# Kernel optimization log

Hardware: AMD Instinct MI355X
Metric: run time of the kernel (lower is better)

The kernel has to match this reference:

```python
import math
import jax, jax.numpy as jnp
import numpy as np

B, SQ, SK, D, H = 4, 2048, 2048, 1024, 16
HD = D // H  # 64


def setup_inputs() -> dict:
    key = jax.random.key(0)
    k1, k2, k3, k4, k5 = jax.random.split(key, 5)
    scale = 1.0 / math.sqrt(D)
    return {
        "hidden_states": jax.random.normal(k1, (B, SQ, D), dtype=jnp.float32),
        "encoder_hidden_states": jax.random.normal(k2, (B, SK, D), dtype=jnp.float32),
        "Wq": jax.random.normal(k3, (D, D), dtype=jnp.float32) * scale,
        "Wk": jax.random.normal(k4, (D, D), dtype=jnp.float32) * scale,
        "Wv": jax.random.normal(k5, (D, D), dtype=jnp.float32) * scale,
    }


def reference(hidden_states, encoder_hidden_states, Wq, Wk, Wv):
    # Linear (bias=False): y = x @ W^T, then split heads -> [B, H, S, HD]
    def split_heads(x, S):
        return x.reshape(B, S, H, HD).transpose(0, 2, 1, 3)

    q = split_heads(hidden_states @ Wq.T, SQ)
    k = split_heads(encoder_hidden_states @ Wk.T, SK)
    v = split_heads(encoder_hidden_states @ Wv.T, SK)

    scores = jnp.einsum("bhqd,bhkd->bhqk", q, k) / math.sqrt(HD)
    probs = jax.nn.softmax(scores, axis=-1)  # no mask, dropout p=0
    ctx = jnp.einsum("bhqk,bhkd->bhqd", probs, v)
    # merge heads -> [B, SQ, D]
    return ctx.transpose(0, 2, 1, 3).reshape(B, SQ, D)
```

## Files before the change

### kernel.cpp

```cpp
#include <hip/hip_runtime.h>
#include <hip/hip_bf16.h>

typedef unsigned short u16;
typedef unsigned int u32;
typedef __attribute__((ext_vector_type(8))) short bf16x8;
typedef __attribute__((ext_vector_type(4))) float f32x4;

#define MFMA32(a, b, c) __builtin_amdgcn_mfma_f32_16x16x32_bf16(a, b, c, 0, 0, 0)

__device__ __forceinline__ float fexp2(float x) { return __builtin_amdgcn_exp2f(x); }

__device__ __forceinline__ u16 f2bf(float f) {
  u32 u = __float_as_uint(f);
  u += 0x7fffu + ((u >> 16) & 1u);
  return (u16)(u >> 16);
}
__device__ __forceinline__ u32 pack2rn(float a, float b) {
  return (u32)f2bf(a) | ((u32)f2bf(b) << 16);
}
__device__ __forceinline__ bf16x8 cvt8(const float4 a, const float4 b) {
  union { bf16x8 v; u32 p[4]; } r;
  r.p[0] = pack2rn(a.x, a.y); r.p[1] = pack2rn(a.z, a.w);
  r.p[2] = pack2rn(b.x, b.y); r.p[3] = pack2rn(b.z, b.w);
  return r.v;
}

__device__ __forceinline__ u32 cvtpk(float lo, float hi) {
  u32 r;
  asm("v_cvt_pk_bf16_f32 %0, %1, %2" : "=v"(r) : "v"(lo), "v"(hi));
  return r;
}
__device__ __forceinline__ void pl32swap(u32& a, u32& b) {
  asm("v_permlane32_swap_b32 %0, %1" : "+v"(a), "+v"(b));
}
__device__ __forceinline__ void pl16swap(u32& a, u32& b) {
  asm("v_permlane16_swap_b32 %0, %1" : "+v"(a), "+v"(b));
}

__device__ __forceinline__ void async_copy16(const void* g, void* l) {
  __builtin_amdgcn_global_load_lds(
      (const __attribute__((address_space(1))) unsigned int*)g,
      (__attribute__((address_space(3))) unsigned int*)l, 16, 0, 0);
}

__global__ __launch_bounds__(256) void cvt_bf16(
    const float* __restrict__ s0, const float* __restrict__ s1,
    const float* __restrict__ s2, const float* __restrict__ s3,
    const float* __restrict__ s4,
    u16* __restrict__ d0, u16* __restrict__ d1, u16* __restrict__ d2,
    u16* __restrict__ d3, u16* __restrict__ d4) {
  const int z = blockIdx.z;
  const float* s = (z == 0) ? s0 : (z == 1) ? s1 : (z == 2) ? s2 : (z == 3) ? s3 : s4;
  u16* d = (z == 0) ? d0 : (z == 1) ? d1 : (z == 2) ? d2 : (z == 3) ? d3 : d4;
  const int n8 = ((z < 2) ? (8192 * 1024) : (1024 * 1024)) / 8;
  const int stride = gridDim.x * 256;
  for (int i = blockIdx.x * 256 + threadIdx.x; i < n8; i += stride) {
    const float4 a = *(const float4*)(s + (size_t)i * 8);
    const float4 b = *(const float4*)(s + (size_t)i * 8 + 4);
    *(bf16x8*)(d + (size_t)i * 8) = cvt8(a, b);
  }
}

__global__ __launch_bounds__(256) void proj_gemm_bf(
    const u16* __restrict__ hb, const u16* __restrict__ eb,
    const u16* __restrict__ wb,
    u16* __restrict__ qb, u16* __restrict__ kb, u16* __restrict__ vt) {
  const int lin = blockIdx.x;
  const int swz = (lin & 7) * 192 + (lin >> 3);
  const int z = swz >> 9;
  const int rem = swz & 511;
  const int m0 = (rem >> 3) * 128;
  const int n0 = (rem & 7) * 128;
  const u16* Ag = (z == 0) ? hb : eb;
  const u16* Bg = wb + (size_t)z * 1024 * 1024;
  __shared__ __attribute__((aligned(16))) u16 Al[128 * 64];
  __shared__ __attribute__((aligned(16))) u16 Bl[128 * 64];
  const int tid = threadIdx.x;
  const int w = tid >> 6, lane = tid & 63;
  const int wm = w >> 1, wn = w & 1;
  const int l15 = lane & 15, quad = lane >> 4;
  const int lr = lane >> 3;
  const int cs8 = ((lane & 7) ^ lr) * 8;
  const int rsw = (l15 & 7) << 3;

  const u16* Ap = Ag + (size_t)(m0 + w * 32 + lr) * 1024 + cs8;
  const u16* Bp = Bg + (size_t)(n0 + w * 32 + lr) * 1024 + cs8;

  f32x4 acc[4][4] = {};

  for (int k0 = 0; k0 < 1024; k0 += 64) {
    __syncthreads();
#pragma unroll
    for (int j = 0; j < 4; j++) {
      async_copy16(Ap + (size_t)j * 8 * 1024 + k0, &Al[(w * 32 + j * 8) * 64]);
      async_copy16(Bp + (size_t)j * 8 * 1024 + k0, &Bl[(w * 32 + j * 8) * 64]);
    }
    __syncthreads();
#pragma unroll
    for (int ks = 0; ks < 2; ks++) {
      bf16x8 af[4], bfr[4];
#pragma unroll
      for (int t = 0; t < 4; t++) {
        af[t] = *(const bf16x8*)&Al[(wm * 64 + t * 16 + l15) * 64 +
                                    ((ks * 32 + quad * 8) ^ rsw)];
        bfr[t] = *(const bf16x8*)&Bl[(wn * 64 + t * 16 + l15) * 64 +
                                     ((ks * 32 + quad * 8) ^ rsw)];
      }
#pragma unroll
      for (int mt = 0; mt < 4; mt++)
#pragma unroll
        for (int nt = 0; nt < 4; nt++)
          acc[mt][nt] = MFMA32(af[mt], bfr[nt], acc[mt][nt]);
    }
  }

  if (z < 2) {
    u16* C = (z == 0) ? qb : kb;
    const float sc = (z == 0) ? 0.18033688011112042f : 1.0f;
#pragma unroll
    for (int mt = 0; mt < 4; mt++)
#pragma unroll
      for (int nt = 0; nt < 4; nt++) {
        const int col = n0 + wn * 64 + nt * 16 + l15;
#pragma unroll
        for (int rr = 0; rr < 4; rr++) {
          const int rowm = m0 + wm * 64 + mt * 16 + quad * 4 + rr;
          C[(size_t)rowm * 1024 + col] = f2bf(acc[mt][nt][rr] * sc);
        }
      }
  } else {
    const int b = m0 >> 11;
#pragma unroll
    for (int mt = 0; mt < 4; mt++) {
      const int key = (m0 & 2047) + wm * 64 + mt * 16 + quad * 4;
#pragma unroll
      for (int nt = 0; nt < 4; nt++) {
        const int n = n0 + wn * 64 + nt * 16 + l15;
        const int h = n >> 6, hd = n & 63;
        uint2 v;
        v.x = pack2rn(acc[mt][nt][0], acc[mt][nt][1]);
        v.y = pack2rn(acc[mt][nt][2], acc[mt][nt][3]);
        *(uint2*)&vt[((size_t)((b * 16 + h) * 64 + hd)) * 2048 + key] = v;
      }
    }
  }
}

__global__ __launch_bounds__(256) void proj_gemm_f32(
    const float* __restrict__ hs, const float* __restrict__ ehs,
    const float* __restrict__ wq, const float* __restrict__ wk,
    const float* __restrict__ wv,
    u16* __restrict__ qb, u16* __restrict__ kb, u16* __restrict__ vt) {
  const int z = blockIdx.z;
  const float* Ag = (z == 0) ? hs : ehs;
  const float* Bg = (z == 0) ? wq : ((z == 1) ? wk : wv);
  const int m0 = blockIdx.y * 128;
  const int n0 = blockIdx.x * 128;
  __shared__ __attribute__((aligned(16))) u16 Al[128 * 40];
  __shared__ __attribute__((aligned(16))) u16 Bl[128 * 40];
  const int tid = threadIdx.x;
  const int w = tid >> 6, lane = tid & 63;
  const int wm = w >> 1, wn = w & 1;
  const int l15 = lane & 15, quad = lane >> 4;
  const int srow = lane >> 2, sch = lane & 3;
  const int r0 = w * 32 + srow, r1 = r0 + 16;

  const float* Ap0 = Ag + (size_t)(m0 + r0) * 1024 + sch * 8;
  const float* Ap1 = Ag + (size_t)(m0 + r1) * 1024 + sch * 8;
  const float* Bp0 = Bg + (size_t)(n0 + r0) * 1024 + sch * 8;
  const float* Bp1 = Bg + (size_t)(n0 + r1) * 1024 + sch * 8;

  f32x4 acc[4][4] = {};

  for (int k0 = 0; k0 < 1024; k0 += 32) {
    const float4 a0l = *(const float4*)(Ap0 + k0), a0h = *(const float4*)(Ap0 + k0 + 4);
    const float4 a1l = *(const float4*)(Ap1 + k0), a1h = *(const float4*)(Ap1 + k0 + 4);
    const float4 b0l = *(const float4*)(Bp0 + k0), b0h = *(const float4*)(Bp0 + k0 + 4);
    const float4 b1l = *(const float4*)(Bp1 + k0), b1h = *(const float4*)(Bp1 + k0 + 4);
    __syncthreads();
    *(bf16x8*)&Al[r0 * 40 + sch * 8] = cvt8(a0l, a0h);
    *(bf16x8*)&Al[r1 * 40 + sch * 8] = cvt8(a1l, a1h);
    *(bf16x8*)&Bl[r0 * 40 + sch * 8] = cvt8(b0l, b0h);
    *(bf16x8*)&Bl[r1 * 40 + sch * 8] = cvt8(b1l, b1h);
    __syncthreads();
    bf16x8 af[4], bfr[4];
#pragma unroll
    for (int t = 0; t < 4; t++) {
      af[t] = *(const bf16x8*)&Al[(wm * 64 + t * 16 + l15) * 40 + quad * 8];
      bfr[t] = *(const bf16x8*)&Bl[(wn * 64 + t * 16 + l15) * 40 + quad * 8];
    }
#pragma unroll
    for (int mt = 0; mt < 4; mt++)
#pragma unroll
      for (int nt = 0; nt < 4; nt++)
        acc[mt][nt] = MFMA32(af[mt], bfr[nt], acc[mt][nt]);
  }

  if (z < 2) {
    u16* C = (z == 0) ? qb : kb;
    const float sc = (z == 0) ? 0.18033688011112042f : 1.0f;
#pragma unroll
    for (int mt = 0; mt < 4; mt++)
#pragma unroll
      for (int nt = 0; nt < 4; nt++) {
        const int col = n0 + wn * 64 + nt * 16 + l15;
#pragma unroll
        for (int rr = 0; rr < 4; rr++) {
          const int rowm = m0 + wm * 64 + mt * 16 + quad * 4 + rr;
          C[(size_t)rowm * 1024 + col] = f2bf(acc[mt][nt][rr] * sc);
        }
      }
  } else {
    const int b = m0 >> 11;
#pragma unroll
    for (int mt = 0; mt < 4; mt++) {
      const int key = (m0 & 2047) + wm * 64 + mt * 16 + quad * 4;
#pragma unroll
      for (int nt = 0; nt < 4; nt++) {
        const int n = n0 + wn * 64 + nt * 16 + l15;
        const int h = n >> 6, hd = n & 63;
        uint2 v;
        v.x = pack2rn(acc[mt][nt][0], acc[mt][nt][1]);
        v.y = pack2rn(acc[mt][nt][2], acc[mt][nt][3]);
        *(uint2*)&vt[((size_t)((b * 16 + h) * 64 + hd)) * 2048 + key] = v;
      }
    }
  }
}

__global__ __launch_bounds__(256, 3) void attn_fwd(
    const u16* __restrict__ qb, const u16* __restrict__ kb,
    const u16* __restrict__ vt, float* __restrict__ out) {
  const int lin = blockIdx.x;
  const int swz = (lin & 7) * 128 + (lin >> 3);
  const int bh = swz >> 4;
  const int b = bh >> 4, h = bh & 15;
  const int q0 = (swz & 15) * 128;
  const int tid = threadIdx.x;
  const int w = tid >> 6, lane = tid & 63;
  const int l15 = lane & 15, quad = lane >> 4;

  __shared__ __attribute__((aligned(16))) u16 Kl[2][64 * 64];
  __shared__ __attribute__((aligned(16))) u16 Vl[2][64 * 64];

  const int wq = w * 32;
  bf16x8 qf[2][2];
#pragma unroll
  for (int nt = 0; nt < 2; nt++)
#pragma unroll
    for (int ks = 0; ks < 2; ks++)
      qf[nt][ks] = *(const bf16x8*)&qb[((size_t)(b * 2048 + q0 + wq + nt * 16 + l15)) * 1024 +
                                       h * 64 + ks * 32 + quad * 8];

  f32x4 o[4][2] = {};
  f32x4 lacc[2] = {};
  const f32x4 z4 = {0.f, 0.f, 0.f, 0.f};
  union { bf16x8 v; u32 p[4]; } one_;
  one_.p[0] = one_.p[1] = one_.p[2] = one_.p[3] = 0x3F803F80u;
  const bf16x8 ones = one_.v;

  const int rsw = (l15 & 7) << 3;
  const int lr = lane >> 3;
  const int cs8 = ((lane & 7) ^ lr) * 8;
  const u16* Kp = kb + ((size_t)(b * 2048 + w * 16 + lr)) * 1024 + h * 64 + cs8;
  const u16* Vp = vt + ((size_t)((b * 16 + h) * 64 + w * 16 + lr)) * 2048 + cs8;

#pragma unroll
  for (int j = 0; j < 2; j++) {
    async_copy16(Kp + (size_t)j * 8 * 1024, &Kl[0][(w * 16 + j * 8) * 64]);
    async_copy16(Vp + (size_t)j * 8 * 2048, &Vl[0][(w * 16 + j * 8) * 64]);
  }

  for (int t = 0; t < 32; ++t) {
    const int cur = t & 1;
    __syncthreads();
    if (t < 31) {
      const size_t ko = (size_t)(t + 1) * 64;
#pragma unroll
      for (int j = 0; j < 2; j++) {
        async_copy16(Kp + (ko + (size_t)j * 8) * 1024,
                     &Kl[cur ^ 1][(w * 16 + j * 8) * 64]);
        async_copy16(Vp + (size_t)j * 8 * 2048 + ko,
                     &Vl[cur ^ 1][(w * 16 + j * 8) * 64]);
      }
    }
    const u16* Kc = Kl[cur];
    const u16* Vc = Vl[cur];

    f32x4 s[4][2];
#pragma unroll
    for (int mt = 0; mt < 4; mt++) {
      const bf16x8 kf = *(const bf16x8*)&Kc[(mt * 16 + l15) * 64 + ((quad * 8) ^ rsw)];
      s[mt][0] = MFMA32(kf, qf[0][0], z4);
      s[mt][1] = MFMA32(kf, qf[1][0], z4);
    }
#pragma unroll
    for (int mt = 0; mt < 4; mt++) {
      const bf16x8 kf =
          *(const bf16x8*)&Kc[(mt * 16 + l15) * 64 + ((32 + quad * 8) ^ rsw)];
      s[mt][0] = MFMA32(kf, qf[0][1], s[mt][0]);
      s[mt][1] = MFMA32(kf, qf[1][1], s[mt][1]);
    }

#pragma unroll
    for (int mt = 0; mt < 4; mt++)
#pragma unroll
      for (int nt = 0; nt < 2; nt++)
#pragma unroll
        for (int rr = 0; rr < 4; rr++)
          s[mt][nt][rr] = fexp2(s[mt][nt][rr]);

#pragma unroll
    for (int kt = 0; kt < 2; kt++) {
      bf16x8 pf[2];
#pragma unroll
      for (int nt = 0; nt < 2; nt++) {
        u32 r00 = cvtpk(s[2 * kt][nt][0], s[2 * kt][nt][1]);
        u32 r01 = cvtpk(s[2 * kt][nt][2], s[2 * kt][nt][3]);
        u32 r10 = cvtpk(s[2 * kt + 1][nt][0], s[2 * kt + 1][nt][1]);
        u32 r11 = cvtpk(s[2 * kt + 1][nt][2], s[2 * kt + 1][nt][3]);
        pl32swap(r00, r10);
        pl32swap(r01, r11);
        pl16swap(r00, r10);
        pl16swap(r01, r11);
        union { bf16x8 v; u32 p[4]; } u;
        u.p[0] = r00; u.p[1] = r01; u.p[2] = r10; u.p[3] = r11;
        pf[nt] = u.v;
      }
      lacc[0] = MFMA32(ones, pf[0], lacc[0]);
      lacc[1] = MFMA32(ones, pf[1], lacc[1]);
#pragma unroll
      for (int ht = 0; ht < 4; ht++) {
        const bf16x8 vf =
            *(const bf16x8*)&Vc[(ht * 16 + l15) * 64 + ((kt * 32 + quad * 8) ^ rsw)];
        o[ht][0] = MFMA32(vf, pf[0], o[ht][0]);
        o[ht][1] = MFMA32(vf, pf[1], o[ht][1]);
      }
    }
  }

#pragma unroll
  for (int nt = 0; nt < 2; nt++) {
    const float rl = 1.0f / lacc[nt][0];
    const size_t rowOff = ((size_t)(b * 2048 + q0 + wq + nt * 16 + l15)) * 1024 + h * 64;
#pragma unroll
    for (int ht = 0; ht < 4; ht++) {
      float4 v;
      v.x = o[ht][nt][0] * rl;
      v.y = o[ht][nt][1] * rl;
      v.z = o[ht][nt][2] * rl;
      v.w = o[ht][nt][3] * rl;
      *(float4*)&out[rowOff + ht * 16 + quad * 4] = v;
    }
  }
}

extern "C" void kernel_launch(void* const* d_in, const int* in_sizes, int n_in,
                              void* d_out, int out_size, void* d_ws, size_t ws_size,
                              hipStream_t stream) {
  const float* hs  = (const float*)d_in[0];
  const float* ehs = (const float*)d_in[1];
  const float* wqp = (const float*)d_in[2];
  const float* wkp = (const float*)d_in[3];
  const float* wvp = (const float*)d_in[4];
  const size_t M8 = (size_t)8192 * 1024;
  u16* qb = (u16*)d_ws;
  u16* kb = qb + M8;
  u16* vt = kb + M8;
  float* ob = (float*)d_out;

  const size_t need = (3 * M8 + 2 * M8 + 3 * (size_t)1024 * 1024) * 2;
  if (ws_size >= need) {
    u16* hb = vt + M8;
    u16* eb = hb + M8;
    u16* wb = eb + M8;
    dim3 gc(512, 1, 5);
    cvt_bf16<<<gc, dim3(256), 0, stream>>>(hs, ehs, wqp, wkp, wvp,
                                           hb, eb, wb, wb + M8 / 8, wb + M8 / 4);
    proj_gemm_bf<<<dim3(1536), dim3(256), 0, stream>>>(hb, eb, wb, qb, kb, vt);
  } else {
    dim3 gg(8, 64, 3);
    proj_gemm_f32<<<gg, dim3(256), 0, stream>>>(hs, ehs, wqp, wkp, wvp, qb, kb, vt);
  }
  attn_fwd<<<dim3(1024), dim3(256), 0, stream>>>(qb, kb, vt, ob);
}
```

Baseline: 249.4 us.

## Double-buffer projection GEMM and use explicit vmcnt waits with MFMA priority

The projection GEMM moves from single-buffered LDS tiles with two syncthreads per k-step to a double-buffered prefetch pipeline, so the next tile's global-to-LDS copy overlaps the current MFMA work. Both the GEMM and the attention loop replace __syncthreads with raw s_barrier plus explicit s_waitcnt vmcnt counts, so only the older copies are waited on. The attention MFMA sections are wrapped in s_setprio to favour matrix issue across waves. The changes double the GEMM's LDS use, which may cut occupancy, and depend on hand-counted vmcnt values being correct.

```diff
diff --git a/kernel.cpp b/kernel.cpp
--- a/kernel.cpp
+++ b/kernel.cpp
@@ -73,8 +73,8 @@
   const int n0 = (rem & 7) * 128;
   const u16* Ag = (z == 0) ? hb : eb;
   const u16* Bg = wb + (size_t)z * 1024 * 1024;
-  __shared__ __attribute__((aligned(16))) u16 Al[128 * 64];
-  __shared__ __attribute__((aligned(16))) u16 Bl[128 * 64];
+  __shared__ __attribute__((aligned(16))) u16 Al[2][128 * 64];
+  __shared__ __attribute__((aligned(16))) u16 Bl[2][128 * 64];
   const int tid = threadIdx.x;
   const int w = tid >> 6, lane = tid & 63;
   const int wm = w >> 1, wn = w & 1;
@@ -88,23 +88,40 @@
 
   f32x4 acc[4][4] = {};
 
-  for (int k0 = 0; k0 < 1024; k0 += 64) {
-    __syncthreads();
-#pragma unroll
-    for (int j = 0; j < 4; j++) {
-      async_copy16(Ap + (size_t)j * 8 * 1024 + k0, &Al[(w * 32 + j * 8) * 64]);
-      async_copy16(Bp + (size_t)j * 8 * 1024 + k0, &Bl[(w * 32 + j * 8) * 64]);
-    }
-    __syncthreads();
+#pragma unroll
+  for (int j = 0; j < 4; j++) {
+    async_copy16(Ap + (size_t)j * 8 * 1024, &Al[0][(w * 32 + j * 8) * 64]);
+    async_copy16(Bp + (size_t)j * 8 * 1024, &Bl[0][(w * 32 + j * 8) * 64]);
+  }
+
+  for (int t = 0; t < 16; ++t) {
+    const int cur = t & 1;
+    __builtin_amdgcn_s_barrier();
+    __builtin_amdgcn_sched_barrier(0);
+    if (t < 15) {
+      const int k0 = (t + 1) * 64;
+#pragma unroll
+      for (int j = 0; j < 4; j++) {
+        async_copy16(Ap + (size_t)j * 8 * 1024 + k0,
+                     &Al[cur ^ 1][(w * 32 + j * 8) * 64]);
+        async_copy16(Bp + (size_t)j * 8 * 1024 + k0,
+                     &Bl[cur ^ 1][(w * 32 + j * 8) * 64]);
+      }
+      asm volatile("s_waitcnt vmcnt(8)" ::: "memory");
+    } else {
+      asm volatile("s_waitcnt vmcnt(0)" ::: "memory");
+    }
+    __builtin_amdgcn_s_barrier();
+    __builtin_amdgcn_sched_barrier(0);
 #pragma unroll
     for (int ks = 0; ks < 2; ks++) {
       bf16x8 af[4], bfr[4];
 #pragma unroll
-      for (int t = 0; t < 4; t++) {
-        af[t] = *(const bf16x8*)&Al[(wm * 64 + t * 16 + l15) * 64 +
-                                    ((ks * 32 + quad * 8) ^ rsw)];
-        bfr[t] = *(const bf16x8*)&Bl[(wn * 64 + t * 16 + l15) * 64 +
-                                     ((ks * 32 + quad * 8) ^ rsw)];
+      for (int t4 = 0; t4 < 4; t4++) {
+        af[t4] = *(const bf16x8*)&Al[cur][(wm * 64 + t4 * 16 + l15) * 64 +
+                                         ((ks * 32 + quad * 8) ^ rsw)];
+        bfr[t4] = *(const bf16x8*)&Bl[cur][(wn * 64 + t4 * 16 + l15) * 64 +
+                                          ((ks * 32 + quad * 8) ^ rsw)];
       }
 #pragma unroll
       for (int mt = 0; mt < 4; mt++)
@@ -273,7 +290,8 @@
 
   for (int t = 0; t < 32; ++t) {
     const int cur = t & 1;
-    __syncthreads();
+    __builtin_amdgcn_s_barrier();
+    __builtin_amdgcn_sched_barrier(0);
     if (t < 31) {
       const size_t ko = (size_t)(t + 1) * 64;
 #pragma unroll
@@ -283,11 +301,17 @@
         async_copy16(Vp + (size_t)j * 8 * 2048 + ko,
                      &Vl[cur ^ 1][(w * 16 + j * 8) * 64]);
       }
-    }
+      asm volatile("s_waitcnt vmcnt(4)" ::: "memory");
+    } else {
+      asm volatile("s_waitcnt vmcnt(0)" ::: "memory");
+    }
+    __builtin_amdgcn_s_barrier();
+    __builtin_amdgcn_sched_barrier(0);
     const u16* Kc = Kl[cur];
     const u16* Vc = Vl[cur];
 
     f32x4 s[4][2];
+    __builtin_amdgcn_s_setprio(1);
 #pragma unroll
     for (int mt = 0; mt < 4; mt++) {
       const bf16x8 kf = *(const bf16x8*)&Kc[(mt * 16 + l15) * 64 + ((quad * 8) ^ rsw)];
@@ -301,6 +325,7 @@
       s[mt][0] = MFMA32(kf, qf[0][1], s[mt][0]);
       s[mt][1] = MFMA32(kf, qf[1][1], s[mt][1]);
     }
+    __builtin_amdgcn_s_setprio(0);
 
 #pragma unroll
     for (int mt = 0; mt < 4; mt++)
@@ -327,6 +352,7 @@
         u.p[0] = r00; u.p[1] = r01; u.p[2] = r10; u.p[3] = r11;
         pf[nt] = u.v;
       }
+      __builtin_amdgcn_s_setprio(1);
       lacc[0] = MFMA32(ones, pf[0], lacc[0]);
       lacc[1] = MFMA32(ones, pf[1], lacc[1]);
 #pragma unroll
@@ -336,6 +362,7 @@
         o[ht][0] = MFMA32(vf, pf[0], o[ht][0]);
         o[ht][1] = MFMA32(vf, pf[1], o[ht][1]);
       }
+      __builtin_amdgcn_s_setprio(0);
     }
   }
 
```

Measured after the change: 255.9 us. +2.6%, slower.

## Fuse fp32-to-bf16 activation conversion into projection GEMM and tune attention barriers

Applied to the files above, without the earlier changes.

The separate conversion pass over hidden_states and encoder_hidden_states is removed. The projection GEMM now reads fp32 activations directly, converts them in registers and stores them swizzled into LDS, prefetching the next K-tile into registers. The attention loop replaces __syncthreads with explicit barriers, partial vmcnt waits and setprio around MFMA blocks to improve overlap. This saves a full write and read of the bf16 activation copies, but the GEMM now reads twice as many A bytes per tile and converts the same A tile once per output column block.

```diff
diff --git a/kernel.cpp b/kernel.cpp
--- a/kernel.cpp
+++ b/kernel.cpp
@@ -43,16 +43,13 @@
       (__attribute__((address_space(3))) unsigned int*)l, 16, 0, 0);
 }
 
-__global__ __launch_bounds__(256) void cvt_bf16(
-    const float* __restrict__ s0, const float* __restrict__ s1,
-    const float* __restrict__ s2, const float* __restrict__ s3,
-    const float* __restrict__ s4,
-    u16* __restrict__ d0, u16* __restrict__ d1, u16* __restrict__ d2,
-    u16* __restrict__ d3, u16* __restrict__ d4) {
+__global__ __launch_bounds__(256) void cvt_w(
+    const float* __restrict__ wq, const float* __restrict__ wk,
+    const float* __restrict__ wv, u16* __restrict__ wb) {
   const int z = blockIdx.z;
-  const float* s = (z == 0) ? s0 : (z == 1) ? s1 : (z == 2) ? s2 : (z == 3) ? s3 : s4;
-  u16* d = (z == 0) ? d0 : (z == 1) ? d1 : (z == 2) ? d2 : (z == 3) ? d3 : d4;
-  const int n8 = ((z < 2) ? (8192 * 1024) : (1024 * 1024)) / 8;
+  const float* s = (z == 0) ? wq : (z == 1) ? wk : wv;
+  u16* d = wb + (size_t)z * 1024 * 1024;
+  const int n8 = (1024 * 1024) / 8;
   const int stride = gridDim.x * 256;
   for (int i = blockIdx.x * 256 + threadIdx.x; i < n8; i += stride) {
     const float4 a = *(const float4*)(s + (size_t)i * 8);
@@ -61,8 +58,8 @@
   }
 }
 
-__global__ __launch_bounds__(256) void proj_gemm_bf(
-    const u16* __restrict__ hb, const u16* __restrict__ eb,
+__global__ __launch_bounds__(256) void proj_gemm_fused(
+    const float* __restrict__ hs, const float* __restrict__ ehs,
     const u16* __restrict__ wb,
     u16* __restrict__ qb, u16* __restrict__ kb, u16* __restrict__ vt) {
   const int lin = blockIdx.x;
@@ -71,7 +68,7 @@
   const int rem = swz & 511;
   const int m0 = (rem >> 3) * 128;
   const int n0 = (rem & 7) * 128;
-  const u16* Ag = (z == 0) ? hb : eb;
+  const float* Ag = (z == 0) ? hs : ehs;
   const u16* Bg = wb + (size_t)z * 1024 * 1024;
   __shared__ __attribute__((aligned(16))) u16 Al[128 * 64];
   __shared__ __attribute__((aligned(16))) u16 Bl[128 * 64];
@@ -83,28 +80,43 @@
   const int cs8 = ((lane & 7) ^ lr) * 8;
   const int rsw = (l15 & 7) << 3;
 
-  const u16* Ap = Ag + (size_t)(m0 + w * 32 + lr) * 1024 + cs8;
   const u16* Bp = Bg + (size_t)(n0 + w * 32 + lr) * 1024 + cs8;
 
+  const int arow = tid >> 1;
+  const int ach = (tid & 1) * 4;
+  const float* Apf = Ag + (size_t)(m0 + arow) * 1024 + ach * 8;
+  const int asw = (arow & 7);
+
   f32x4 acc[4][4] = {};
-
-  for (int k0 = 0; k0 < 1024; k0 += 64) {
+  float4 a[8];
+#pragma unroll
+  for (int j = 0; j < 8; j++) a[j] = *(const float4*)(Apf + j * 4);
+
+  for (int t = 0; t < 16; ++t) {
+    const int k0 = t * 64;
     __syncthreads();
 #pragma unroll
-    for (int j = 0; j < 4; j++) {
-      async_copy16(Ap + (size_t)j * 8 * 1024 + k0, &Al[(w * 32 + j * 8) * 64]);
+    for (int cc = 0; cc < 4; cc++)
+      *(bf16x8*)&Al[arow * 64 + (((ach + cc) ^ asw) * 8)] =
+          cvt8(a[2 * cc], a[2 * cc + 1]);
+#pragma unroll
+    for (int j = 0; j < 4; j++)
       async_copy16(Bp + (size_t)j * 8 * 1024 + k0, &Bl[(w * 32 + j * 8) * 64]);
-    }
     __syncthreads();
+    if (t < 15) {
+#pragma unroll
+      for (int j = 0; j < 8; j++)
+        a[j] = *(const float4*)(Apf + k0 + 64 + j * 4);
+    }
 #pragma unroll
     for (int ks = 0; ks < 2; ks++) {
       bf16x8 af[4], bfr[4];
 #pragma unroll
-      for (int t = 0; t < 4; t++) {
-        af[t] = *(const bf16x8*)&Al[(wm * 64 + t * 16 + l15) * 64 +
-                                    ((ks * 32 + quad * 8) ^ rsw)];
-        bfr[t] = *(const bf16x8*)&Bl[(wn * 64 + t * 16 + l15) * 64 +
+      for (int t4 = 0; t4 < 4; t4++) {
+        af[t4] = *(const bf16x8*)&Al[(wm * 64 + t4 * 16 + l15) * 64 +
                                      ((ks * 32 + quad * 8) ^ rsw)];
+        bfr[t4] = *(const bf16x8*)&Bl[(wn * 64 + t4 * 16 + l15) * 64 +
+                                      ((ks * 32 + quad * 8) ^ rsw)];
       }
 #pragma unroll
       for (int mt = 0; mt < 4; mt++)
@@ -273,7 +285,8 @@
 
   for (int t = 0; t < 32; ++t) {
     const int cur = t & 1;
-    __syncthreads();
+    __builtin_amdgcn_s_barrier();
+    __builtin_amdgcn_sched_barrier(0);
     if (t < 31) {
       const size_t ko = (size_t)(t + 1) * 64;
 #pragma unroll
@@ -283,11 +296,17 @@
         async_copy16(Vp + (size_t)j * 8 * 2048 + ko,
                      &Vl[cur ^ 1][(w * 16 + j * 8) * 64]);
       }
-    }
+      asm volatile("s_waitcnt vmcnt(4)" ::: "memory");
+    } else {
+      asm volatile("s_waitcnt vmcnt(0)" ::: "memory");
+    }
+    __builtin_amdgcn_s_barrier();
+    __builtin_amdgcn_sched_barrier(0);
     const u16* Kc = Kl[cur];
     const u16* Vc = Vl[cur];
 
     f32x4 s[4][2];
+    __builtin_amdgcn_s_setprio(1);
 #pragma unroll
     for (int mt = 0; mt < 4; mt++) {
       const bf16x8 kf = *(const bf16x8*)&Kc[(mt * 16 + l15) * 64 + ((quad * 8) ^ rsw)];
@@ -301,6 +320,7 @@
       s[mt][0] = MFMA32(kf, qf[0][1], s[mt][0]);
       s[mt][1] = MFMA32(kf, qf[1][1], s[mt][1]);
     }
+    __builtin_amdgcn_s_setprio(0);
 
 #pragma unroll
     for (int mt = 0; mt < 4; mt++)
@@ -327,6 +347,7 @@
         u.p[0] = r00; u.p[1] = r01; u.p[2] = r10; u.p[3] = r11;
         pf[nt] = u.v;
       }
+      __builtin_amdgcn_s_setprio(1);
       lacc[0] = MFMA32(ones, pf[0], lacc[0]);
       lacc[1] = MFMA32(ones, pf[1], lacc[1]);
 #pragma unroll
@@ -336,6 +357,7 @@
         o[ht][0] = MFMA32(vf, pf[0], o[ht][0]);
         o[ht][1] = MFMA32(vf, pf[1], o[ht][1]);
       }
+      __builtin_amdgcn_s_setprio(0);
     }
   }
 
@@ -367,17 +389,13 @@
   u16* qb = (u16*)d_ws;
   u16* kb = qb + M8;
   u16* vt = kb + M8;
+  u16* wb = vt + M8;
   float* ob = (float*)d_out;
 
-  const size_t need = (3 * M8 + 2 * M8 + 3 * (size_t)1024 * 1024) * 2;
+  const size_t need = (3 * M8 + 3 * (size_t)1024 * 1024) * 2;
   if (ws_size >= need) {
-    u16* hb = vt + M8;
-    u16* eb = hb + M8;
-    u16* wb = eb + M8;
-    dim3 gc(512, 1, 5);
-    cvt_bf16<<<gc, dim3(256), 0, stream>>>(hs, ehs, wqp, wkp, wvp,
-                                           hb, eb, wb, wb + M8 / 8, wb + M8 / 4);
-    proj_gemm_bf<<<dim3(1536), dim3(256), 0, stream>>>(hb, eb, wb, qb, kb, vt);
+    cvt_w<<<dim3(128, 1, 3), dim3(256), 0, stream>>>(wqp, wkp, wvp, wb);
+    proj_gemm_fused<<<dim3(1536), dim3(256), 0, stream>>>(hs, ehs, wb, qb, kb, vt);
   } else {
     dim3 gg(8, 64, 3);
     proj_gemm_f32<<<gg, dim3(256), 0, stream>>>(hs, ehs, wqp, wkp, wvp, qb, kb, vt);
```

Measured after the change: 313.2 us. 25.6% more time.
